# Optimization experiments

Measured on AMD Instinct MI355X. Metric: run time of the kernel, lower is better.

## Reference

```python
import jax, jax.numpy as jnp
import numpy as np

EPS = 1e-5
NHEAD = 8
NEG = -1e9  # matches -inf masked-fill semantics; rows never fully masked after fallback


def layer_norm(x, g, b):
    m = jnp.mean(x, axis=-1, keepdims=True)
    v = jnp.var(x, axis=-1, keepdims=True)
    return (x - m) * jax.lax.rsqrt(v + EPS) * g + b


def mha(q, k, v, Wqkv, bqkv, Wo, bo, bias=None):
    # torch nn.MultiheadAttention math (batch_first). Wqkv: [C, 3C] (jax layout).
    B, N, C = q.shape
    M = k.shape[1]
    d = C // NHEAD
    Wq, Wk, Wv = jnp.split(Wqkv, 3, axis=1)
    bq, bk, bv = jnp.split(bqkv, 3)
    qp = (q @ Wq + bq).reshape(B, N, NHEAD, d)
    kp = (k @ Wk + bk).reshape(B, M, NHEAD, d)
    vp = (v @ Wv + bv).reshape(B, M, NHEAD, d)
    s = jnp.einsum('bnhd,bmhd->bhnm', qp, kp) / np.sqrt(d).astype(q.dtype)
    if bias is not None:
        s = s + bias  # [B,1,N,M] broadcast over heads
    a = jax.nn.softmax(s, axis=-1)
    o = jnp.einsum('bhnm,bmhd->bnhd', a, vp).reshape(B, N, C)
    return o @ Wo + bo


def setup_inputs() -> dict:
    key = jax.random.key(0)
    B, Nq, HW, C, F = 8, 100, 4096, 512, 2048
    ks = jax.random.split(key, 16)
    s = 0.02
    inp = {
        'q': jax.random.normal(ks[0], (B, Nq, C), jnp.float32),
        'kv': jax.random.normal(ks[1], (B, HW, C), jnp.float32),
        'mask_bin': jax.random.randint(ks[2], (B, Nq, HW), 0, 2, jnp.int32),
        # MaskedXAttn: attn params + norm_q/norm_kv
        'xa_Wqkv': jax.random.normal(ks[3], (C, 3 * C), jnp.float32) * s,
        'xa_bqkv': jnp.zeros((3 * C,), jnp.float32),
        'xa_Wo': jax.random.normal(ks[4], (C, C), jnp.float32) * s,
        'xa_bo': jnp.zeros((C,), jnp.float32),
        'xa_gq': jnp.ones((C,), jnp.float32),
        'xa_bq_ln': jnp.zeros((C,), jnp.float32),
        'xa_gkv': jnp.ones((C,), jnp.float32),
        'xa_bkv_ln': jnp.zeros((C,), jnp.float32),
        # self-attention
        'sa_Wqkv': jax.random.normal(ks[5], (C, 3 * C), jnp.float32) * s,
        'sa_bqkv': jnp.zeros((3 * C,), jnp.float32),
        'sa_Wo': jax.random.normal(ks[6], (C, C), jnp.float32) * s,
        'sa_bo': jnp.zeros((C,), jnp.float32),
        # norms
        'n1_g': jnp.ones((C,), jnp.float32), 'n1_b': jnp.zeros((C,), jnp.float32),
        'n2_g': jnp.ones((C,), jnp.float32), 'n2_b': jnp.zeros((C,), jnp.float32),
        # FFN (MLP with num_layers=2: Linear(C,F), ReLU, Linear(F,C))
        'ff_W1': jax.random.normal(ks[7], (C, F), jnp.float32) * s,
        'ff_b1': jnp.zeros((F,), jnp.float32),
        'ff_W2': jax.random.normal(ks[8], (F, C), jnp.float32) * s,
        'ff_b2': jnp.zeros((C,), jnp.float32),
    }
    return inp


def reference(q, kv, mask_bin,
              xa_Wqkv, xa_bqkv, xa_Wo, xa_bo, xa_gq, xa_bq_ln, xa_gkv, xa_bkv_ln,
              sa_Wqkv, sa_bqkv, sa_Wo, sa_bo,
              n1_g, n1_b, n2_g, n2_b,
              ff_W1, ff_b1, ff_W2, ff_b2):
    # --- masked cross-attention (vectorized equivalent of per-query loop) ---
    qn = layer_norm(q, xa_gq, xa_bq_ln)
    kvn = layer_norm(kv, xa_gkv, xa_bkv_ln)
    allow = mask_bin.astype(bool)                      # [B,Nq,HW] True = attend
    row_any = jnp.any(allow, axis=-1, keepdims=True)   # queries with empty mask -> full attention
    eff = jnp.where(row_any, allow, True)
    bias = jnp.where(eff, 0.0, NEG).astype(q.dtype)[:, None, :, :]  # [B,1,Nq,HW]
    xa = mha(qn, kvn, kvn, xa_Wqkv, xa_bqkv, xa_Wo, xa_bo, bias=bias)
    q = q + xa
    # --- self-attention over queries ---
    qn1 = layer_norm(q, n1_g, n1_b)
    sa = mha(qn1, qn1, qn1, sa_Wqkv, sa_bqkv, sa_Wo, sa_bo)
    q = q + sa
    # --- FFN ---
    qn2 = layer_norm(q, n2_g, n2_b)
    h = jax.nn.relu(qn2 @ ff_W1 + ff_b1)
    q = q + (h @ ff_W2 + ff_b2)
    return q
```

## Files before the change

kernel.cpp:

```cpp
#include <hip/hip_runtime.h>

typedef unsigned short u16;
typedef unsigned int u32;
typedef __bf16 bf16x8 __attribute__((ext_vector_type(8)));
typedef short s16x4 __attribute__((ext_vector_type(4)));
typedef float f32x4 __attribute__((ext_vector_type(4)));

#define NEG_INF -3.0e38f
#define QSCALE 0.18033688011f

__device__ __forceinline__ u16 f2bf(float f){
  union { float f; u32 u; } v; v.f = f;
  u32 r = v.u + 0x7fffu + ((v.u >> 16) & 1u);
  return (u16)(r >> 16);
}
__device__ __forceinline__ float bf2f(u16 h){
  union { u32 u; float f; } v; v.u = ((u32)h) << 16; return v.f;
}
__device__ __forceinline__ short f2bf_s(float f){
  union { __bf16 h; short s; } cv; cv.h = (__bf16)f; return cv.s;
}

__device__ __forceinline__ f32x4 mfma16(s16x4 a, s16x4 b, f32x4 c){
#if __has_builtin(__builtin_amdgcn_mfma_f32_16x16x16bf16_1k)
  return __builtin_amdgcn_mfma_f32_16x16x16bf16_1k(a, b, c, 0, 0, 0);
#else
  asm("v_mfma_f32_16x16x16_bf16 %0, %1, %2, %0" : "+v"(c) : "v"(a), "v"(b));
  return c;
#endif
}

__device__ __forceinline__ void gl_lds16(const void* g, void* l){
  __builtin_amdgcn_global_load_lds((const __attribute__((address_space(1))) void*)g,
      (__attribute__((address_space(3))) void*)l, 16, 0, 0);
}

__device__ __forceinline__ void ln_body(const float* __restrict__ xr,
    const float* __restrict__ g, const float* __restrict__ b,
    u16* __restrict__ orow, int lane){
  float4 v0 = *(const float4*)(xr + lane * 4);
  float4 v1 = *(const float4*)(xr + 256 + lane * 4);
  float s = v0.x+v0.y+v0.z+v0.w + v1.x+v1.y+v1.z+v1.w;
  float q = v0.x*v0.x+v0.y*v0.y+v0.z*v0.z+v0.w*v0.w
          + v1.x*v1.x+v1.y*v1.y+v1.z*v1.z+v1.w*v1.w;
  #pragma unroll
  for (int d=1; d<64; d<<=1){ s += __shfl_xor(s, d, 64); q += __shfl_xor(q, d, 64); }
  float mean = s * (1.0f/512.0f);
  float var  = q * (1.0f/512.0f) - mean*mean;
  float rs = rsqrtf(var + 1e-5f);
  float4 g0 = *(const float4*)(g + lane*4), g1 = *(const float4*)(g + 256 + lane*4);
  float4 b0 = *(const float4*)(b + lane*4), b1 = *(const float4*)(b + 256 + lane*4);
  uint2 pa, pb;
  pa.x = (u32)f2bf((v0.x-mean)*rs*g0.x + b0.x) | ((u32)f2bf((v0.y-mean)*rs*g0.y + b0.y) << 16);
  pa.y = (u32)f2bf((v0.z-mean)*rs*g0.z + b0.z) | ((u32)f2bf((v0.w-mean)*rs*g0.w + b0.w) << 16);
  pb.x = (u32)f2bf((v1.x-mean)*rs*g1.x + b1.x) | ((u32)f2bf((v1.y-mean)*rs*g1.y + b1.y) << 16);
  pb.y = (u32)f2bf((v1.z-mean)*rs*g1.z + b1.z) | ((u32)f2bf((v1.w-mean)*rs*g1.w + b1.w) << 16);
  *(uint2*)(orow + lane*4) = pa;
  *(uint2*)(orow + 256 + lane*4) = pb;
}

__global__ __launch_bounds__(256) void ln_rows(const float* __restrict__ x,
    const float* __restrict__ g, const float* __restrict__ b,
    u16* __restrict__ out, int rows){
  int wid = threadIdx.x >> 6, lane = threadIdx.x & 63;
  int row = blockIdx.x * 4 + wid;
  if (row >= rows) return;
  ln_body(x + (size_t)row*512, g, b, out + (size_t)row*512, lane);
}

struct WtJobs {
  const float* W[7]; u16* Wt[7];
  int K[7], Nfull[7], ncol0[7], nt[7], blk0[7];
};
struct PrepArgs {
  WtJobs wt; int totW;
  const float *x0, *g0, *b0; u16* o0; int nb0, rows0;
  const float *x1, *g1, *b1; u16* o1; int nb1, rows1;
  const int* mask; u32* mw;
};

__global__ __launch_bounds__(256) void prep_all(PrepArgs P){
  __shared__ float tile[32][33];
  __shared__ unsigned long long blds[4];
  int bb = blockIdx.x;
  int tid = threadIdx.x;
  int wid = tid >> 6, lane = tid & 63;
  if (bb < P.totW){
    const WtJobs& J = P.wt;
    const float* W = J.W[0]; u16* Wt = J.Wt[0];
    int K = J.K[0], Nfull = J.Nfull[0], ncol0 = J.ncol0[0], nt = J.nt[0], blk0 = 0;
    #pragma unroll
    for (int i=1;i<7;i++)
      if (bb >= J.blk0[i]){
        W=J.W[i]; Wt=J.Wt[i]; K=J.K[i]; Nfull=J.Nfull[i]; ncol0=J.ncol0[i]; nt=J.nt[i]; blk0=J.blk0[i];
      }
    int lb = bb - blk0;
    int tk = lb / nt, tn = lb % nt;
    int col = tid & 31, kr = tid >> 5;
    #pragma unroll
    for (int i=0;i<4;i++){
      int k = tk*32 + kr + i*8;
      tile[kr + i*8][col] = W[(size_t)k*Nfull + ncol0 + tn*32 + col];
    }
    __syncthreads();
    int nl = tid >> 3, kc = (tid & 7) * 4;
    uint2 o;
    o.x = (u32)f2bf(tile[kc+0][nl]) | ((u32)f2bf(tile[kc+1][nl]) << 16);
    o.y = (u32)f2bf(tile[kc+2][nl]) | ((u32)f2bf(tile[kc+3][nl]) << 16);
    *(uint2*)(Wt + (size_t)(tn*32 + nl)*K + tk*32 + kc) = o;
  } else if (bb < P.totW + P.nb0){
    int row = (bb - P.totW)*4 + wid;
    if (row >= P.rows0) return;
    ln_body(P.x0 + (size_t)row*512, P.g0, P.b0, P.o0 + (size_t)row*512, lane);
  } else if (bb < P.totW + P.nb0 + P.nb1){
    int row = (bb - P.totW - P.nb0)*4 + wid;
    if (row >= P.rows1) return;
    ln_body(P.x1 + (size_t)row*512, P.g1, P.b1, P.o1 + (size_t)row*512, lane);
  } else {
    int lb = bb - P.totW - P.nb0 - P.nb1;
    int r0 = lb*2 + (wid >> 1);
    int word = tid & 127;
    const int* mr = P.mask + (size_t)r0*4096 + word*32;
    u32 w = 0;
    #pragma unroll
    for (int j=0;j<32;j+=4){
      int4 v = *(const int4*)(mr + j);
      w |= (u32)(v.x!=0) << j;
      w |= (u32)(v.y!=0) << (j+1);
      w |= (u32)(v.z!=0) << (j+2);
      w |= (u32)(v.w!=0) << (j+3);
    }
    blds[wid] = __ballot(w != 0);
    __syncthreads();
    bool any = (wid < 2) ? ((blds[0] | blds[1]) != 0ull) : ((blds[2] | blds[3]) != 0ull);
    P.mw[(size_t)r0*128 + word] = any ? w : 0xffffffffu;
  }
}

struct GemmJob {
  const u16* A; const u16* Bt; const float* bias;
  float* outf; u16* outb; const float* res; u16* out2;
  int M, N, K, lda, k0, ksplit, scale_cols, T1, rows_per_b, vstride, swz, brmap, blk0, nblk;
};
struct GemmJobs { GemmJob j[2]; int njobs; };

template<int EPI>
__device__ __forceinline__ void epi_store(const GemmJob& J, f32x4 (&acc)[4][4],
    int m0, int n0, int wm, int wn, int lg, int l15, int ksp){
  if (EPI == 3){
    float bv[4];
    #pragma unroll
    for (int ni=0;ni<4;ni++) bv[ni] = J.bias[n0 + wn*64 + ni*16 + l15];
    #pragma unroll
    for (int ni=0;ni<4;ni++){
      int c = n0 + wn*64 + ni*16 + l15;
      #pragma unroll
      for (int mi=0;mi<4;mi++){
        int mr0 = m0 + wm*64 + mi*16 + lg*4;
        if (mr0 >= J.M) continue;
        if (c < J.T1){
          #pragma unroll
          for (int r4=0;r4<4;r4++)
            J.outb[(size_t)(mr0+r4)*J.T1 + c] = f2bf(acc[mi][ni][r4] + bv[ni]);
        } else {
          int bidx = mr0 / J.rows_per_b;
          int key  = mr0 - bidx*J.rows_per_b;
          uint2 o;
          o.x = (u32)f2bf(acc[mi][ni][0]+bv[ni]) | ((u32)f2bf(acc[mi][ni][1]+bv[ni])<<16);
          o.y = (u32)f2bf(acc[mi][ni][2]+bv[ni]) | ((u32)f2bf(acc[mi][ni][3]+bv[ni])<<16);
          *(uint2*)(J.out2 + ((size_t)bidx*512 + (c - J.T1))*J.vstride + key) = o;
        }
      }
    }
  } else if (EPI == 4){
    #pragma unroll
    for (int mi=0;mi<4;mi++){
      #pragma unroll
      for (int r4=0;r4<4;r4++){
        int m = m0 + wm*64 + mi*16 + lg*4 + r4;
        if (m >= J.M) continue;
        float rb = J.bias[m];
        #pragma unroll
        for (int ni=0;ni<4;ni++){
          int c = n0 + wn*64 + ni*16 + l15;
          J.outb[(size_t)m*J.N + c] = f2bf(acc[mi][ni][r4] + rb);
        }
      }
    }
  } else if (EPI == 5){
    float* po_ = J.outf + (size_t)ksp*J.M*J.N;
    #pragma unroll
    for (int mi=0;mi<4;mi++){
      #pragma unroll
      for (int r4=0;r4<4;r4++){
        int m = m0 + wm*64 + mi*16 + lg*4 + r4;
        if (m >= J.M) continue;
        #pragma unroll
        for (int ni=0;ni<4;ni++){
          int c = n0 + wn*64 + ni*16 + l15;
          po_[(size_t)m*J.N + c] = acc[mi][ni][r4];
        }
      }
    }
  } else {
    float bv[4], scl[4];
    #pragma unroll
    for (int ni=0;ni<4;ni++){
      int c = n0 + wn*64 + ni*16 + l15;
      bv[ni]  = J.bias[c];
      scl[ni] = (c < J.scale_cols) ? QSCALE : 1.0f;
    }
    #pragma unroll
    for (int mi=0;mi<4;mi++){
      #pragma unroll
      for (int r4=0;r4<4;r4++){
        int m = m0 + wm*64 + mi*16 + lg*4 + r4;
        if (m >= J.M) continue;
        #pragma unroll
        for (int ni=0;ni<4;ni++){
          int c = n0 + wn*64 + ni*16 + l15;
          float v = acc[mi][ni][r4] + bv[ni];
          if (EPI == 0){
            J.outb[(size_t)m*J.N + c] = f2bf(v*scl[ni]);
          } else if (EPI == 1){
            J.outb[(size_t)m*J.N + c] = f2bf(fmaxf(v, 0.0f));
          } else {
            J.outf[(size_t)m*J.N + c] = v + J.res[(size_t)m*J.N + c];
          }
        }
      }
    }
  }
}

template<int EPI>
__device__ __forceinline__ void gemm_block(const GemmJob& J, int bidIn, u16* As, u16* Bs){
  int bid = bidIn;
  int ksp = 0;
  if (J.ksplit > 1){ ksp = bid / J.nblk; bid = bid % J.nblk; }
  if (J.swz){ int cpx = J.nblk >> 3; bid = (bid & 7)*cpx + (bid >> 3); }
  int NT = J.N >> 7;
  int mt = bid / NT, nt = bid % NT;
  int m0 = mt << 7, n0 = nt << 7;
  int kofs = J.k0 + ksp * J.K;
  int tid = threadIdx.x;
  int wid = tid >> 6, lane = tid & 63;
  int wm = wid >> 1, wn = wid & 1;
  int lg = lane >> 4, l15 = lane & 15;

  f32x4 acc[4][4] = {};
  int ktiles = J.K >> 6;
  for (int kt = 0; kt < ktiles; ++kt){
    int k0 = kofs + (kt << 6);
    if (kt) __syncthreads();
    #pragma unroll
    for (int i=0;i<4;i++){
      int L = i*4096 + tid*16;
      int T = L ^ (((L>>7)&7)<<4);
      int row = T >> 7, colb = T & 127;
      int ga = m0 + row; if (ga > J.M-1) ga = J.M-1;
      gl_lds16((const char*)J.A + ((size_t)ga*J.lda + k0)*2 + colb, (char*)As + L);
    }
    #pragma unroll
    for (int i=0;i<4;i++){
      int L = i*4096 + tid*16;
      int T = L ^ (((L>>7)&7)<<4);
      int row = T >> 7, colb = T & 127;
      int rowg = n0 + row;
      if (J.brmap){ int rb = rowg & 127; rowg = (rowg>>7)*J.brmap + (rb < J.brmap ? rb : J.brmap-1); }
      gl_lds16((const char*)J.Bt + ((size_t)rowg*J.lda + k0)*2 + colb, (char*)Bs + L);
    }
    __syncthreads();
    #pragma unroll
    for (int ks=0; ks<2; ++ks){
      bf16x8 af[4], bfr[4];
      #pragma unroll
      for (int mi=0; mi<4; ++mi){
        int r = wm*64 + mi*16 + l15;
        int byt = r*128 + ks*64 + lg*16;
        af[mi] = *(const bf16x8*)((const char*)As + (byt ^ ((r&7)<<4)));
      }
      #pragma unroll
      for (int ni=0; ni<4; ++ni){
        int r = wn*64 + ni*16 + l15;
        int byt = r*128 + ks*64 + lg*16;
        bfr[ni] = *(const bf16x8*)((const char*)Bs + (byt ^ ((r&7)<<4)));
      }
      __builtin_amdgcn_s_setprio(1);
      #pragma unroll
      for (int mi=0;mi<4;mi++)
        #pragma unroll
        for (int ni=0;ni<4;ni++)
          acc[mi][ni] = __builtin_amdgcn_mfma_f32_16x16x32_bf16(af[mi], bfr[ni], acc[mi][ni], 0,0,0);
      __builtin_amdgcn_s_setprio(0);
    }
  }
  epi_store<EPI>(J, acc, m0, n0, wm, wn, lg, l15, ksp);
}

template<int EPIA, int EPIB>
__global__ __launch_bounds__(256) void gemm_multi(GemmJobs G){
  __shared__ __align__(16) u16 As[8192];
  __shared__ __align__(16) u16 Bs[8192];
  bool second = (G.njobs > 1) && ((int)blockIdx.x >= G.j[1].blk0);
  if (second) gemm_block<EPIB>(G.j[1], (int)blockIdx.x - G.j[1].blk0, As, Bs);
  else        gemm_block<EPIA>(G.j[0], (int)blockIdx.x, As, Bs);
}

__global__ __launch_bounds__(256) void splitk_reduce(
    const float* __restrict__ part, int nsplit, const float* __restrict__ bias,
    const float* __restrict__ res, float* __restrict__ out, int N, int total4)
{
  int idx = (blockIdx.x*256 + threadIdx.x);
  if (idx >= total4) return;
  int e0 = idx*4;
  size_t MN = (size_t)total4*4;
  float4 a = *(const float4*)(part + e0);
  #pragma unroll
  for (int s=1;s<4;s++){
    float4 p = *(const float4*)(part + s*MN + e0);
    a.x += p.x; a.y += p.y; a.z += p.z; a.w += p.w;
  }
  float4 r = *(const float4*)(res + e0);
  int c = e0 & (N-1);
  float4 bv = *(const float4*)(bias + c);
  float4 o;
  o.x = a.x + r.x + bv.x; o.y = a.y + r.y + bv.y;
  o.z = a.z + r.z + bv.z; o.w = a.w + r.w + bv.w;
  *(float4*)(out + e0) = o;
}

template<bool PARTIAL, bool HASMASK, int NTILES>
__global__ __launch_bounds__(256) void attn_kernel(
    const u16* __restrict__ Qp, int ldq,
    const u16* __restrict__ Kp, int ldk, int kcol0,
    const u16* __restrict__ VT, size_t vbs, int vfs,
    const u32* __restrict__ maskw,
    float* __restrict__ pm, float* __restrict__ pl, u16* __restrict__ po,
    u16* __restrict__ o_out,
    int nq, int mk, int S, int H, int Bp, int swz)
{
  __shared__ __align__(16) u16 Ks[2*4096];
  __shared__ __align__(16) u16 Vs[2*4096];
  int bid = blockIdx.x;
  if (swz){ int cpx = gridDim.x >> 3; bid = (bid & 7)*cpx + (bid >> 3); }
  int s = bid % S; int h = (bid / S) % H; int b = bid / (S*H);
  int tid = threadIdx.x, wid = tid>>6, lane = tid&63;
  int lg = lane>>4, l15 = lane&15;
  int qbase = b*nq;
  int kps = mk / S;
  int kbeg = s * kps;
  int mwld = mk >> 5;
  int krel = lg*4;

  bf16x8 qf[2][2];
  #pragma unroll
  for (int mt=0;mt<2;mt++){
    int qr = wid*32 + mt*16 + l15; int qc = qr < nq ? qr : nq-1;
    #pragma unroll
    for (int ks=0;ks<2;ks++)
      qf[mt][ks] = *(const bf16x8*)(Qp + (size_t)(qbase+qc)*ldq + h*64 + ks*32 + lg*8);
  }
  u32 wmw[2][2*NTILES];
  if (HASMASK){
    #pragma unroll
    for (int mt=0;mt<2;mt++){
      int qc = (wid*32 + mt*16 + l15) < nq ? (wid*32 + mt*16 + l15) : nq-1;
      const u32* mrow = maskw + (size_t)(qbase+qc)*mwld + (kbeg>>5);
      #pragma unroll
      for (int wi=0; wi<2*NTILES; wi+=4){
        uint4 v = *(const uint4*)(mrow + wi);
        wmw[mt][wi+0]=v.x; wmw[mt][wi+1]=v.y; wmw[mt][wi+2]=v.z; wmw[mt][wi+3]=v.w;
      }
    }
  }

  float m_r[2] = {NEG_INF, NEG_INF};
  float l_r[2] = {0.0f, 0.0f};
  f32x4 of[2][4] = {};

  auto stage = [&](int t_, int bufi){
    int kb_ = kbeg + t_*64;
    #pragma unroll
    for (int i=0;i<2;i++){
      int idx = i*256 + tid;
      int key = idx>>3, sd = idx&7;
      int kc = kb_ + key; if (kc > mk-1) kc = mk-1;
      const char* src = (const char*)(Kp + (size_t)(b*mk + kc)*ldk + kcol0 + h*64) + ((sd ^ (key&7))<<4);
      gl_lds16(src, (char*)Ks + bufi*8192 + idx*16);
    }
    #pragma unroll
    for (int i=0;i<2;i++){
      int idx = i*256 + tid;
      int f = idx>>3, sd = idx&7;
      const char* src = (const char*)(VT + (size_t)b*vbs + (size_t)(h*64+f)*vfs + kb_) + ((sd ^ (f&7))<<4);
      gl_lds16(src, (char*)Vs + bufi*8192 + idx*16);
    }
  };

  stage(0, 0);

  #pragma unroll
  for (int t=0;t<NTILES;t++){
    if (t+1 < NTILES){
      stage(t+1, (t+1)&1);
      asm volatile("s_waitcnt vmcnt(4)" ::: "memory");
    } else {
      asm volatile("s_waitcnt vmcnt(0)" ::: "memory");
    }
    __builtin_amdgcn_s_barrier();

    const char* Kb = (const char*)Ks + (t&1)*8192;
    const char* Vb = (const char*)Vs + (t&1)*8192;
    int kb = kbeg + t*64;

    f32x4 sT[4][2] = {};
    #pragma unroll
    for (int nt2=0;nt2<4;nt2++){
      bf16x8 k0 = *(const bf16x8*)(Kb + ((nt2*16+l15)<<7) + (((lg  ) ^ (l15&7))<<4));
      bf16x8 k1 = *(const bf16x8*)(Kb + ((nt2*16+l15)<<7) + (((4+lg) ^ (l15&7))<<4));
      __builtin_amdgcn_s_setprio(1);
      #pragma unroll
      for (int mt=0;mt<2;mt++){
        sT[nt2][mt] = __builtin_amdgcn_mfma_f32_16x16x32_bf16(k0, qf[mt][0], sT[nt2][mt], 0,0,0);
        sT[nt2][mt] = __builtin_amdgcn_mfma_f32_16x16x32_bf16(k1, qf[mt][1], sT[nt2][mt], 0,0,0);
      }
      __builtin_amdgcn_s_setprio(0);
    }

    s16x4 pb[2][4];
    #pragma unroll
    for (int mt=0;mt<2;mt++){
      float mx = NEG_INF;
      #pragma unroll
      for (int nt2=0;nt2<4;nt2++){
        u32 wb = 0;
        if (HASMASK) wb = wmw[mt][t*2 + (nt2>>1)] >> (((nt2&1)<<4) + krel);
        #pragma unroll
        for (int r=0;r<4;r++){
          bool ok = HASMASK ? (((wb>>r)&1u) != 0) : (kb + nt2*16 + krel + r < mk);
          float sv = ok ? sT[nt2][mt][r] : NEG_INF;
          sT[nt2][mt][r] = sv;
          mx = fmaxf(mx, sv);
        }
      }
      mx = fmaxf(mx, __shfl_xor(mx, 16, 64));
      mx = fmaxf(mx, __shfl_xor(mx, 32, 64));
      if (!__all(mx <= m_r[mt] + 8.0f)){
        float mnew = fmaxf(m_r[mt], mx);
        float corr = exp2f(m_r[mt] - mnew);
        m_r[mt] = mnew;
        l_r[mt] *= corr;
        #pragma unroll
        for (int nf=0;nf<4;nf++) of[mt][nf] *= corr;
      }
      float ps = 0.0f;
      #pragma unroll
      for (int nt2=0;nt2<4;nt2++)
        #pragma unroll
        for (int r=0;r<4;r++){
          float p = exp2f(sT[nt2][mt][r] - m_r[mt]);
          ps += p;
          pb[mt][nt2][r] = f2bf_s(p);
        }
      ps += __shfl_xor(ps, 16, 64);
      ps += __shfl_xor(ps, 32, 64);
      l_r[mt] += ps;
    }

    #pragma unroll
    for (int nf=0;nf<4;nf++){
      s16x4 vf[4];
      #pragma unroll
      for (int nt2=0;nt2<4;nt2++){
        int slot = (nt2*2 + (lg>>1)) ^ (l15&7);
        vf[nt2] = *(const s16x4*)(Vb + ((nf*16+l15)<<7) + (slot<<4) + ((lg&1)<<3));
      }
      __builtin_amdgcn_s_setprio(1);
      #pragma unroll
      for (int mt=0;mt<2;mt++)
        #pragma unroll
        for (int nt2=0;nt2<4;nt2++)
          of[mt][nf] = mfma16(vf[nt2], pb[mt][nt2], of[mt][nf]);
      __builtin_amdgcn_s_setprio(0);
    }
    __builtin_amdgcn_s_barrier();
  }

  #pragma unroll
  for (int mt=0;mt<2;mt++){
    int q = wid*32 + mt*16 + l15;
    if (q < nq){
      if (PARTIAL){
        size_t base = (((size_t)(s*Bp + b)*H + h)*128 + q);
        if (lg == 0){ pm[base] = m_r[mt]; pl[base] = l_r[mt]; }
        #pragma unroll
        for (int nf=0;nf<4;nf++){
          uint2 o;
          o.x = (u32)f2bf(of[mt][nf][0]) | ((u32)f2bf(of[mt][nf][1])<<16);
          o.y = (u32)f2bf(of[mt][nf][2]) | ((u32)f2bf(of[mt][nf][3])<<16);
          *(uint2*)(po + base*64 + nf*16 + lg*4) = o;
        }
      } else {
        float inv = 1.0f / l_r[mt];
        #pragma unroll
        for (int nf=0;nf<4;nf++){
          uint2 o;
          o.x = (u32)f2bf(of[mt][nf][0]*inv) | ((u32)f2bf(of[mt][nf][1]*inv)<<16);
          o.y = (u32)f2bf(of[mt][nf][2]*inv) | ((u32)f2bf(of[mt][nf][3]*inv)<<16);
          *(uint2*)(o_out + (size_t)(qbase+q)*512 + h*64 + nf*16 + lg*4) = o;
        }
      }
    }
  }
}

__global__ __launch_bounds__(64) void attn_combine(
    const float* __restrict__ pm, const float* __restrict__ pl, const u16* __restrict__ po,
    u16* __restrict__ o_out, int S, int Bp, int H, int nq)
{
  int bid = blockIdx.x;
  int q = bid % nq; int h = (bid / nq) % H; int b = bid / (nq*H);
  int f = threadIdx.x;
  float mstar = NEG_INF;
  for (int s=0;s<S;s++){
    size_t idx = (((size_t)(s*Bp + b)*H + h)*128 + q);
    mstar = fmaxf(mstar, pm[idx]);
  }
  float L = 0.0f, acc = 0.0f;
  for (int s=0;s<S;s++){
    size_t idx = (((size_t)(s*Bp + b)*H + h)*128 + q);
    float w = exp2f(pm[idx] - mstar);
    L += w * pl[idx];
    acc += w * bf2f(po[idx*64 + f]);
  }
  o_out[((size_t)b*nq + q)*512 + h*64 + f] = f2bf(acc / L);
}

extern "C" void kernel_launch(void* const* d_in, const int* in_sizes, int n_in,
                              void* d_out, int out_size, void* d_ws, size_t ws_size,
                              hipStream_t stream){
  const float* q_in    = (const float*)d_in[0];
  const float* kv_in   = (const float*)d_in[1];
  const int*   maskb   = (const int*)d_in[2];
  const float* xa_Wqkv = (const float*)d_in[3];
  const float* xa_bqkv = (const float*)d_in[4];
  const float* xa_Wo   = (const float*)d_in[5];
  const float* xa_bo   = (const float*)d_in[6];
  const float* xa_gq   = (const float*)d_in[7];
  const float* xa_bq   = (const float*)d_in[8];
  const float* xa_gkv  = (const float*)d_in[9];
  const float* xa_bkv  = (const float*)d_in[10];
  const float* sa_Wqkv = (const float*)d_in[11];
  const float* sa_bqkv = (const float*)d_in[12];
  const float* sa_Wo   = (const float*)d_in[13];
  const float* sa_bo   = (const float*)d_in[14];
  const float* n1_g = (const float*)d_in[15];
  const float* n1_b = (const float*)d_in[16];
  const float* n2_g = (const float*)d_in[17];
  const float* n2_b = (const float*)d_in[18];
  const float* ff_W1 = (const float*)d_in[19];
  const float* ff_b1 = (const float*)d_in[20];
  const float* ff_W2 = (const float*)d_in[21];
  const float* ff_b2 = (const float*)d_in[22];

  char* ws = (char*)d_ws;
  size_t off = 0;
  auto alloc = [&](size_t bytes)->char*{ char* p = ws + off; off = (off + bytes + 255) & ~(size_t)255; return p; };
  u16* wq  = (u16*)alloc((size_t)512*512*2);
  u16* wkv = (u16*)alloc((size_t)1024*512*2);
  u16* wsa = (u16*)alloc((size_t)1536*512*2);
  u16* wxo = (u16*)alloc((size_t)512*512*2);
  u16* wso = (u16*)alloc((size_t)512*512*2);
  u16* wf1 = (u16*)alloc((size_t)2048*512*2);
  u16* wf2 = (u16*)alloc((size_t)512*2048*2);
  u16* qn  = (u16*)alloc((size_t)800*512*2);
  u16* qp  = (u16*)alloc((size_t)800*512*2);
  u32* mw  = (u32*)alloc((size_t)800*128*4);
  u16* kp  = (u16*)alloc((size_t)32768*512*2);
  u16* vpT = (u16*)alloc((size_t)8*512*4096*2);
  size_t reuse_off = off;
  u16* kvn = (u16*)alloc((size_t)32768*512*2);
  size_t offB = reuse_off;
  auto allocB = [&](size_t bytes)->char*{ char* p = ws + offB; offB = (offB + bytes + 255) & ~(size_t)255; return p; };
  const int S = 16;
  float* pm   = (float*)allocB((size_t)S*64*128*4);
  float* pl   = (float*)allocB((size_t)S*64*128*4);
  u16*   po   = (u16*)allocB((size_t)S*64*128*64*2);
  u16* o_xa   = (u16*)allocB((size_t)800*512*2);
  float* x1   = (float*)allocB((size_t)800*512*4);
  u16* qn1    = (u16*)allocB((size_t)800*512*2);
  u16* saqkv  = (u16*)allocB((size_t)800*1024*2);
  u16* vT2sa  = (u16*)allocB((size_t)512*1024*2);
  u16* o_sa   = (u16*)allocB((size_t)800*512*2);
  float* x2   = (float*)allocB((size_t)800*512*4);
  u16* qn2    = (u16*)allocB((size_t)800*512*2);
  u16* hbuf   = (u16*)allocB((size_t)800*2048*2);
  float* fpart = pm;

  PrepArgs P;
  P.wt.W[0]=xa_Wqkv; P.wt.Wt[0]=wq;  P.wt.K[0]=512;  P.wt.Nfull[0]=1536; P.wt.ncol0[0]=0;   P.wt.nt[0]=16;
  P.wt.W[1]=xa_Wqkv; P.wt.Wt[1]=wkv; P.wt.K[1]=512;  P.wt.Nfull[1]=1536; P.wt.ncol0[1]=512; P.wt.nt[1]=32;
  P.wt.W[2]=sa_Wqkv; P.wt.Wt[2]=wsa; P.wt.K[2]=512;  P.wt.Nfull[2]=1536; P.wt.ncol0[2]=0;   P.wt.nt[2]=48;
  P.wt.W[3]=xa_Wo;   P.wt.Wt[3]=wxo; P.wt.K[3]=512;  P.wt.Nfull[3]=512;  P.wt.ncol0[3]=0;   P.wt.nt[3]=16;
  P.wt.W[4]=sa_Wo;   P.wt.Wt[4]=wso; P.wt.K[4]=512;  P.wt.Nfull[4]=512;  P.wt.ncol0[4]=0;   P.wt.nt[4]=16;
  P.wt.W[5]=ff_W1;   P.wt.Wt[5]=wf1; P.wt.K[5]=512;  P.wt.Nfull[5]=2048; P.wt.ncol0[5]=0;   P.wt.nt[5]=64;
  P.wt.W[6]=ff_W2;   P.wt.Wt[6]=wf2; P.wt.K[6]=2048; P.wt.Nfull[6]=512;  P.wt.ncol0[6]=0;   P.wt.nt[6]=16;
  int tot = 0;
  for (int i=0;i<7;i++){ P.wt.blk0[i] = tot; tot += (P.wt.K[i]/32)*P.wt.nt[i]; }
  P.totW = tot;
  P.x0=q_in;  P.g0=xa_gq;  P.b0=xa_bq;  P.o0=qn;  P.nb0=200;  P.rows0=800;
  P.x1=kv_in; P.g1=xa_gkv; P.b1=xa_bkv; P.o1=kvn; P.nb1=8192; P.rows1=32768;
  P.mask=maskb; P.mw=mw;
  prep_all<<<tot + 200 + 8192 + 400, 256, 0, stream>>>(P);

  auto mkjob = [&](const u16*A, const u16*Bt, const float*bias, float*outf, u16*outb,
                   const float*res, u16*out2, int M, int N, int K, int lda, int k0,
                   int ksplit, int sc, int T1, int rpb, int vst, int swz, int brm,
                   int blk0, int nblk)->GemmJob{
    GemmJob j; j.A=A; j.Bt=Bt; j.bias=bias; j.outf=outf; j.outb=outb; j.res=res; j.out2=out2;
    j.M=M; j.N=N; j.K=K; j.lda=lda; j.k0=k0; j.ksplit=ksplit; j.scale_cols=sc; j.T1=T1;
    j.rows_per_b=rpb; j.vstride=vst; j.swz=swz; j.brmap=brm; j.blk0=blk0; j.nblk=nblk;
    return j;
  };

  {
    GemmJobs g;
    g.j[0] = mkjob(qn, wq, xa_bqkv, nullptr, qp, nullptr, nullptr,
                   800, 512, 512, 512, 0, 1, 512, 0,1,1, 0,0, 0, 28);
    g.j[1] = mkjob(kvn, wkv, xa_bqkv+512, nullptr, kp, nullptr, vpT,
                   32768, 1024, 512, 512, 0, 1, 0, 512, 4096, 4096, 1, 0, 28, 2048);
    g.njobs = 2;
    gemm_multi<0,3><<<28 + 2048, 256, 0, stream>>>(g);
  }
  attn_kernel<true,true,4><<<8*8*S, 256, 0, stream>>>(
      qp, 512, kp, 512, 0, vpT, (size_t)512*4096, 4096, mw,
      pm, pl, po, nullptr, 100, 4096, S, 8, 8, 1);
  attn_combine<<<8*8*100, 64, 0, stream>>>(pm, pl, po, o_xa, S, 8, 8, 100);
  {
    GemmJobs g;
    g.j[0] = mkjob(o_xa, wxo, xa_bo, x1, nullptr, q_in, nullptr,
                   800, 512, 512, 512, 0, 1, 0, 0,1,1, 0,0, 0, 28);
    g.j[1] = g.j[0]; g.njobs = 1;
    gemm_multi<2,2><<<28, 256, 0, stream>>>(g);
  }
  ln_rows<<<200, 256, 0, stream>>>(x1, n1_g, n1_b, qn1, 800);
  {
    GemmJobs g;
    g.j[0] = mkjob(qn1, wsa, sa_bqkv, nullptr, saqkv, nullptr, nullptr,
                   800, 1024, 512, 512, 0, 1, 512, 0,1,1, 0,0, 0, 56);
    g.j[1] = mkjob(wsa + (size_t)1024*512, qn1, sa_bqkv+1024, nullptr, vT2sa, nullptr, nullptr,
                   512, 1024, 512, 512, 0, 1, 0, 0,1,1, 0, 100, 56, 32);
    g.njobs = 2;
    gemm_multi<0,4><<<56 + 32, 256, 0, stream>>>(g);
  }
  attn_kernel<false,false,2><<<64, 256, 0, stream>>>(
      saqkv, 1024, saqkv, 1024, 512, vT2sa, (size_t)128, 1024, nullptr,
      nullptr, nullptr, nullptr, o_sa, 100, 100, 1, 8, 8, 0);
  {
    GemmJobs g;
    g.j[0] = mkjob(o_sa, wso, sa_bo, x2, nullptr, x1, nullptr,
                   800, 512, 512, 512, 0, 1, 0, 0,1,1, 0,0, 0, 28);
    g.j[1] = g.j[0]; g.njobs = 1;
    gemm_multi<2,2><<<28, 256, 0, stream>>>(g);
  }
  ln_rows<<<200, 256, 0, stream>>>(x2, n2_g, n2_b, qn2, 800);
  {
    GemmJobs g;
    g.j[0] = mkjob(qn2, wf1, ff_b1, nullptr, hbuf, nullptr, nullptr,
                   800, 2048, 512, 512, 0, 1, 0, 0,1,1, 0,0, 0, 112);
    g.j[1] = g.j[0]; g.njobs = 1;
    gemm_multi<1,1><<<112, 256, 0, stream>>>(g);
  }
  {
    GemmJobs g;
    g.j[0] = mkjob(hbuf, wf2, nullptr, fpart, nullptr, nullptr, nullptr,
                   800, 512, 512, 2048, 0, 4, 0, 0,1,1, 0,0, 0, 28);
    g.j[1] = g.j[0]; g.njobs = 1;
    gemm_multi<5,5><<<112, 256, 0, stream>>>(g);
  }
  splitk_reduce<<<(800*512/4 + 255)/256, 256, 0, stream>>>(
      fpart, 4, ff_b2, x2, (float*)d_out, 512, 800*512/4);
}
```

Baseline: 225.1 us.

## Add 256x256-tile GEMM kernel for cross-attention Q/KV projections

Replaces the generic 256-thread multi-job GEMM for the cross-attention Q and fused K/V projections with a new 512-thread kernel using 256x256 output tiles. It uses 128KB of LDS with double-buffered, XOR-swizzled K-halves and explicit vmcnt waits, plus a grouped block swizzle for the large KV job. Bigger tiles raise arithmetic intensity and reuse of A and B per block for the 32768x1024x512 GEMM. In exchange it adds more register pressure per thread, and the 800-row Q job now runs as 8 large mostly-idle tiles.

```diff
diff --git a/kernel.cpp b/kernel.cpp
--- a/kernel.cpp
+++ b/kernel.cpp
@@ -305,6 +305,135 @@
   bool second = (G.njobs > 1) && ((int)blockIdx.x >= G.j[1].blk0);
   if (second) gemm_block<EPIB>(G.j[1], (int)blockIdx.x - G.j[1].blk0, As, Bs);
   else        gemm_block<EPIA>(G.j[0], (int)blockIdx.x, As, Bs);
+}
+
+struct G256Job {
+  const u16* A; const u16* Bt; const float* bias;
+  u16* outb; u16* out2;
+  int M, N, lda, epi, nblk, swz;
+};
+
+__global__ __launch_bounds__(512, 2) void gemm256(G256Job J0, G256Job J1, int blk1, int njobs){
+  __shared__ __align__(16) char lds[131072];
+  G256Job J = J0;
+  int lb = blockIdx.x;
+  if (njobs > 1 && lb >= blk1){ J = J1; lb -= blk1; }
+  if (J.swz){ int cpx = J.nblk >> 3; lb = (lb & 7)*cpx + (lb >> 3); }
+  int NT = J.N >> 8;
+  int mt = lb / NT, nt = lb % NT;
+  int m0 = mt << 8, n0 = nt << 8;
+  int tid = threadIdx.x;
+  int wid = tid >> 6, lane = tid & 63;
+  int wm = wid >> 2, wn = wid & 3;
+  int lg = lane >> 4, l15 = lane & 15;
+  const int KT = 8;
+  char* Al = lds;
+  char* Bl = lds + 65536;
+
+  auto stage_pair = [&](int t, int h){
+    int bufo = ((t & 1) << 15) | (h << 14);
+    #pragma unroll
+    for (int i=0;i<2;i++){
+      int idx = i*512 + tid;
+      int row = idx >> 2, s = idx & 3;
+      int sg = s ^ (row & 3);
+      int ga = m0 + row; if (ga > J.M-1) ga = J.M-1;
+      gl_lds16((const char*)J.A + ((size_t)ga*J.lda + t*64 + h*32 + sg*8)*2,
+               Al + bufo + idx*16);
+    }
+    #pragma unroll
+    for (int i=0;i<2;i++){
+      int idx = i*512 + tid;
+      int row = idx >> 2, s = idx & 3;
+      int sg = s ^ (row & 3);
+      gl_lds16((const char*)J.Bt + ((size_t)(n0 + row)*J.lda + t*64 + h*32 + sg*8)*2,
+               Bl + bufo + idx*16);
+    }
+  };
+
+  f32x4 acc[8][4] = {};
+  stage_pair(0, 0);
+  stage_pair(0, 1);
+  for (int t=0; t<KT; ++t){
+    #pragma unroll
+    for (int h=0; h<2; ++h){
+      if (t+1 < KT){
+        stage_pair(t+1, h);
+        asm volatile("s_waitcnt vmcnt(8)" ::: "memory");
+      } else if (h == 0){
+        asm volatile("s_waitcnt vmcnt(4)" ::: "memory");
+      } else {
+        asm volatile("s_waitcnt vmcnt(0)" ::: "memory");
+      }
+      __builtin_amdgcn_s_barrier();
+      int bufo = ((t & 1) << 15) | (h << 14);
+      bf16x8 af[8], bfr[4];
+      #pragma unroll
+      for (int ni=0;ni<4;ni++){
+        int row = wn*64 + ni*16 + l15;
+        bfr[ni] = *(const bf16x8*)(Bl + bufo + row*64 + ((lg ^ (row&3))<<4));
+      }
+      #pragma unroll
+      for (int mi=0;mi<8;mi++){
+        int row = wm*128 + mi*16 + l15;
+        af[mi] = *(const bf16x8*)(Al + bufo + row*64 + ((lg ^ (row&3))<<4));
+      }
+      __builtin_amdgcn_s_setprio(1);
+      #pragma unroll
+      for (int mi=0;mi<8;mi++)
+        #pragma unroll
+        for (int ni=0;ni<4;ni++)
+          acc[mi][ni] = __builtin_amdgcn_mfma_f32_16x16x32_bf16(af[mi], bfr[ni], acc[mi][ni], 0,0,0);
+      __builtin_amdgcn_s_setprio(0);
+      __builtin_amdgcn_s_barrier();
+    }
+  }
+
+  float bv[4];
+  #pragma unroll
+  for (int ni=0;ni<4;ni++) bv[ni] = J.bias[n0 + wn*64 + ni*16 + l15];
+  if (J.epi == 0){
+    #pragma unroll
+    for (int mi=0;mi<8;mi++){
+      #pragma unroll
+      for (int r=0;r<4;r++){
+        int m = m0 + wm*128 + mi*16 + lg*4 + r;
+        if (m >= J.M) continue;
+        #pragma unroll
+        for (int ni=0;ni<4;ni++){
+          int c = n0 + wn*64 + ni*16 + l15;
+          J.outb[(size_t)m*J.N + c] = f2bf((acc[mi][ni][r] + bv[ni])*QSCALE);
+        }
+      }
+    }
+  } else if (n0 < 512){
+    #pragma unroll
+    for (int mi=0;mi<8;mi++){
+      #pragma unroll
+      for (int r=0;r<4;r++){
+        int m = m0 + wm*128 + mi*16 + lg*4 + r;
+        #pragma unroll
+        for (int ni=0;ni<4;ni++){
+          int c = n0 + wn*64 + ni*16 + l15;
+          J.outb[(size_t)m*512 + c] = f2bf(acc[mi][ni][r] + bv[ni]);
+        }
+      }
+    }
+  } else {
+    #pragma unroll
+    for (int ni=0;ni<4;ni++){
+      int f = n0 - 512 + wn*64 + ni*16 + l15;
+      #pragma unroll
+      for (int mi=0;mi<8;mi++){
+        int m = m0 + wm*128 + mi*16 + lg*4;
+        int bidx = m >> 12, key = m & 4095;
+        uint2 o;
+        o.x = (u32)f2bf(acc[mi][ni][0]+bv[ni]) | ((u32)f2bf(acc[mi][ni][1]+bv[ni])<<16);
+        o.y = (u32)f2bf(acc[mi][ni][2]+bv[ni]) | ((u32)f2bf(acc[mi][ni][3]+bv[ni])<<16);
+        *(uint2*)(J.out2 + ((size_t)bidx*512 + f)*4096 + key) = o;
+      }
+    }
+  }
 }
 
 __global__ __launch_bounds__(256) void splitk_reduce(
@@ -625,13 +754,12 @@
   };
 
   {
-    GemmJobs g;
-    g.j[0] = mkjob(qn, wq, xa_bqkv, nullptr, qp, nullptr, nullptr,
-                   800, 512, 512, 512, 0, 1, 512, 0,1,1, 0,0, 0, 28);
-    g.j[1] = mkjob(kvn, wkv, xa_bqkv+512, nullptr, kp, nullptr, vpT,
-                   32768, 1024, 512, 512, 0, 1, 0, 512, 4096, 4096, 1, 0, 28, 2048);
-    g.njobs = 2;
-    gemm_multi<0,3><<<28 + 2048, 256, 0, stream>>>(g);
+    G256Job jkv, jq;
+    jkv.A = kvn; jkv.Bt = wkv; jkv.bias = xa_bqkv+512; jkv.outb = kp; jkv.out2 = vpT;
+    jkv.M = 32768; jkv.N = 1024; jkv.lda = 512; jkv.epi = 3; jkv.nblk = 512; jkv.swz = 1;
+    jq.A = qn; jq.Bt = wq; jq.bias = xa_bqkv; jq.outb = qp; jq.out2 = nullptr;
+    jq.M = 800; jq.N = 512; jq.lda = 512; jq.epi = 0; jq.nblk = 8; jq.swz = 0;
+    gemm256<<<512 + 8, 512, 0, stream>>>(jkv, jq, 512, 2);
   }
   attn_kernel<true,true,4><<<8*8*S, 256, 0, stream>>>(
       qp, 512, kp, 512, 0, vpT, (size_t)512*4096, 4096, mw,
```

Result: slower. 233.2 us (+3.6%).
